# Performance work log

Measured on AMD Instinct MI355X. Metric: run time of the kernel, lower is better.

## Reference

```python
import jax, jax.numpy as jnp
import numpy as np

DC_WZ = 15
ETA = 0.1
RADIUS = DC_WZ // 2  # 7
EPS = 1e-3


def avg_pool2d(x, k, pad):
    # torch F.avg_pool2d default: zero padding, count_include_pad=True -> divide by k*k always
    s = jax.lax.reduce_window(
        x, 0.0, jax.lax.add,
        window_dimensions=(1, 1, k, k),
        window_strides=(1, 1, 1, 1),
        padding=[(0, 0), (0, 0), (pad, pad), (pad, pad)])
    return s / float(k * k)


def min_pool2d_replicate(x, k, pad):
    # replicate (edge) pad then VALID min-pool, matching -max_pool2d(-pad(x, replicate))
    xp = jnp.pad(x, ((0, 0), (0, 0), (pad, pad), (pad, pad)), mode='edge')
    return jax.lax.reduce_window(
        xp, jnp.inf, jax.lax.min,
        window_dimensions=(1, 1, k, k),
        window_strides=(1, 1, 1, 1),
        padding='VALID')


def guided_filter(guide, src, radius, eps=EPS):
    k = 2 * radius + 1
    mean_I = avg_pool2d(guide, k, radius)
    mean_p = avg_pool2d(src, k, radius)
    mean_Ip = avg_pool2d(guide * src, k, radius)
    cov_Ip = mean_Ip - mean_I * mean_p
    mean_II = avg_pool2d(guide * guide, k, radius)
    var_I = mean_II - mean_I * mean_I
    a = cov_Ip / (var_I + eps)
    b = mean_p - a * mean_I
    mean_a = avg_pool2d(a, k, radius)
    mean_b = avg_pool2d(b, k, radius)
    return mean_a * guide + mean_b


def setup_inputs() -> dict:
    key = jax.random.key(0)
    k1, k2 = jax.random.split(key)
    smoky_image = jax.random.uniform(k1, (16, 3, 512, 512), dtype=jnp.float32)
    rho_DNN = jax.random.uniform(k2, (16, 3, 512, 512), dtype=jnp.float32)
    return {"smoky_image": smoky_image, "rho_DNN": rho_DNN}


def reference(smoky_image, rho_DNN):
    # dark channel: per-pixel min over RGB, then 15x15 min-pool with replicate pad
    dc_pixel = jnp.min(smoky_image, axis=-3, keepdims=True)  # [B,1,H,W]
    dc_coarse = min_pool2d_replicate(dc_pixel, DC_WZ, RADIUS)
    guide_I = jnp.mean(smoky_image, axis=-3, keepdims=True)
    dc_refined = guided_filter(guide_I, dc_coarse, RADIUS, EPS)
    dc_refined = jax.lax.stop_gradient(dc_refined)  # torch: no_grad + detach
    dc_rho = (ETA + dc_refined) / (ETA + 1.0) * (1.0 - rho_DNN)
    return smoky_image - dc_rho
```

## Files before the change

kernel.cpp:

```cpp
#include <hip/hip_runtime.h>

#define BATCH 16
#define HH 512
#define WW 512
#define PLANE (HH*WW)

#define LDS_WAIT()   asm volatile("s_waitcnt lgkmcnt(0)" ::: "memory")
#define WAVE_FENCE() asm volatile("" ::: "memory")

__device__ __forceinline__ float bf_lo(unsigned u) {
    union { unsigned u; float f; } c; c.u = u << 16; return c.f;
}
__device__ __forceinline__ float bf_hi(unsigned u) {
    union { unsigned u; float f; } c; c.u = u & 0xFFFF0000u; return c.f;
}
__device__ __forceinline__ unsigned f2bf(float f) {
    union { float f; unsigned u; } c; c.f = f;
    return (c.u + 0x7FFFu + ((c.u >> 16) & 1u)) >> 16;
}
__device__ __forceinline__ unsigned packbf(float x, float y) {
    return f2bf(x) | (f2bf(y) << 16);
}
__device__ __forceinline__ float min3f(float a, float b, float c) {
    return fminf(fminf(a, b), c);
}

#define T1 64
#define HALO 7
#define LW (T1 + 2*HALO)

__global__ __launch_bounds__(256) void k1_guide_minpool(
    const float* __restrict__ smoky, unsigned* __restrict__ gp)
{
    __shared__ float dcp[LW*LW];
    __shared__ float vmn[T1*LW];
    __shared__ unsigned short gsh[T1*T1];
    int nwg = gridDim.x;
    int wg = (blockIdx.x & 7) * (nwg >> 3) + (blockIdx.x >> 3);
    int img  = wg >> 6;
    int tile = wg & 63;
    int y0 = (tile >> 3) * T1;
    int x0 = (tile & 7) * T1;
    int t = threadIdx.x;
    const float* s0 = smoky + (size_t)img * 3 * PLANE;
    unsigned* gpl = gp + (size_t)img * PLANE;

    for (int i = t; i < LW*LW; i += 256) {
        int ly = i / LW, lx = i - ly * LW;
        int iy = y0 - HALO + ly, ix = x0 - HALO + lx;
        int cy = min(max(iy, 0), HH-1);
        int cx = min(max(ix, 0), WW-1);
        const float* bp = s0 + cy * WW + cx;
        float c0 = bp[0], c1 = bp[PLANE], c2 = bp[2*PLANE];
        dcp[i] = min3f(c0, c1, c2);
        if (ly >= HALO && ly < HALO+T1 && lx >= HALO && lx < HALO+T1)
            gsh[(ly-HALO)*T1 + (lx-HALO)] = (unsigned short)f2bf((c0 + c1 + c2) * (1.0f/3.0f));
    }
    __syncthreads();
    for (int i = t; i < T1*LW; i += 256) {
        int r = i / LW, c = i - r * LW;
        const float* q = &dcp[r*LW + c];
        float m = min3f(min3f(min3f(q[0*LW],q[1*LW],q[2*LW]),
                              min3f(q[3*LW],q[4*LW],q[5*LW]),
                              min3f(q[6*LW],q[7*LW],q[8*LW])),
                        min3f(q[9*LW],q[10*LW],q[11*LW]),
                        min3f(q[12*LW],q[13*LW],q[14*LW]));
        vmn[i] = m;
    }
    __syncthreads();
    for (int i = t; i < T1*T1; i += 256) {
        int r = i >> 6, c = i & 63;
        const float* q = &vmn[r*LW + c];
        float m = min3f(min3f(min3f(q[0],q[1],q[2]),
                              min3f(q[3],q[4],q[5]),
                              min3f(q[6],q[7],q[8])),
                        min3f(q[9],q[10],q[11]),
                        min3f(q[12],q[13],q[14]));
        gpl[(y0+r)*WW + x0 + c] = (unsigned)gsh[r*T1+c] | (f2bf(m) << 16);
    }
}

#define RS2 8

__global__ __launch_bounds__(256) void k2_ab(
    const unsigned* __restrict__ gp, unsigned* __restrict__ abO)
{
    __shared__ float2 eo[4][4][80];
    int nwg = gridDim.x;
    int wg = (blockIdx.x & 7) * (nwg >> 3) + (blockIdx.x >> 3);
    int w = threadIdx.x >> 6, l = threadIdx.x & 63;
    int gw = wg * 4 + w;
    int img   = gw >> 8;
    int cg    = (gw >> 6) & 3;
    int strip = gw & 63;
    int y0 = strip * RS2;
    int c0 = cg * 128;
    const unsigned* gpP = gp + (size_t)img * PLANE;
    unsigned* abP = abO + (size_t)img * PLANE;

    int cm = c0 + 2*l;
    int hj = l & 3;
    int hcol  = (l < 4) ? (c0 - 8 + 2*hj) : (c0 + 128 + 2*hj);
    bool hv   = (l < 8) && (hcol >= 0) && (hcol < WW);
    int hslot = (l < 4) ? hj : (68 + hj);

    float sI[2]={0,0}, sII[2]={0,0}, sPv[2]={0,0}, sIp[2]={0,0};
    float hI[2]={0,0}, hII[2]={0,0}, hPv[2]={0,0}, hIp[2]={0,0};

    auto loadrow = [&](int y, uint2& um, uint2& uh) {
        int yc = min(max(y, 0), HH-1);
        const unsigned* r = gpP + (size_t)yc * WW;
        uint2 a = *reinterpret_cast<const uint2*>(r + cm);
        uint2 b = make_uint2(0u, 0u);
        if (hv) b = *reinterpret_cast<const uint2*>(r + hcol);
        bool rv = ((unsigned)y < (unsigned)HH);
        um.x = rv ? a.x : 0u;  um.y = rv ? a.y : 0u;
        uh.x = rv ? b.x : 0u;  uh.y = rv ? b.y : 0u;
    };

    for (int r = y0 - 8; r <= y0 + 6; ++r) {
        uint2 um, uh; loadrow(r, um, uh);
        unsigned mm[2]={um.x,um.y}, hh[2]={uh.x,uh.y};
        #pragma unroll
        for (int k = 0; k < 2; ++k) {
            float g=bf_lo(mm[k]), p=bf_hi(mm[k]);
            sI[k]+=g; sII[k]+=g*g; sPv[k]+=p; sIp[k]+=g*p;
            float gh=bf_lo(hh[k]), ph=bf_hi(hh[k]);
            hI[k]+=gh; hII[k]+=gh*gh; hPv[k]+=ph; hIp[k]+=gh*ph;
        }
    }
    uint2 adM, adH, sbM, sbH;
    loadrow(y0 + 7, adM, adH);
    loadrow(y0 - 8, sbM, sbH);

    float2* EO = &eo[w][0][0];
    const float inv225 = 1.0f/225.0f;
    for (int y = y0; y < y0 + RS2; ++y) {
        {
            unsigned am[2]={adM.x,adM.y}, sm[2]={sbM.x,sbM.y};
            unsigned ah[2]={adH.x,adH.y}, sh[2]={sbH.x,sbH.y};
            #pragma unroll
            for (int k = 0; k < 2; ++k) {
                float gA=bf_lo(am[k]), pA=bf_hi(am[k]);
                float gS=bf_lo(sm[k]), pS=bf_hi(sm[k]);
                sI[k]+=gA-gS; sII[k]+=gA*gA-gS*gS; sPv[k]+=pA-pS; sIp[k]+=gA*pA-gS*pS;
                float gAh=bf_lo(ah[k]), pAh=bf_hi(ah[k]);
                float gSh=bf_lo(sh[k]), pSh=bf_hi(sh[k]);
                hI[k]+=gAh-gSh; hII[k]+=gAh*gAh-gSh*gSh; hPv[k]+=pAh-pSh; hIp[k]+=gAh*pAh-gSh*pSh;
            }
        }
        loadrow(y + 8, adM, adH);
        loadrow(y - 7, sbM, sbH);
        EO[l+4]       = make_float2(sI[0],  sI[1]);
        EO[80 + l+4]  = make_float2(sII[0], sII[1]);
        EO[160 + l+4] = make_float2(sPv[0], sPv[1]);
        EO[240 + l+4] = make_float2(sIp[0], sIp[1]);
        if (l < 8) {
            EO[hslot]       = make_float2(hI[0],  hI[1]);
            EO[80 + hslot]  = make_float2(hII[0], hII[1]);
            EO[160 + hslot] = make_float2(hPv[0], hPv[1]);
            EO[240 + hslot] = make_float2(hIp[0], hIp[1]);
        }
        LDS_WAIT();
        float S0[4], S1[4];
        #pragma unroll
        for (int q = 0; q < 4; ++q) {
            float2 t[9];
            #pragma unroll
            for (int m = 0; m < 9; ++m) t[m] = EO[q*80 + l + m];
            float so = ((t[0].y+t[1].y)+(t[2].y+t[3].y)) + ((t[4].y+t[5].y)+(t[6].y+t[7].y));
            float se = ((t[1].x+t[2].x)+(t[3].x+t[4].x)) + ((t[5].x+t[6].x)+t[7].x);
            S0[q] = so + se;
            S1[q] = S0[q] - t[0].y + t[8].x;
        }
        WAVE_FENCE();
        unsigned pk0, pk1;
        {
            float mI = S0[0]*inv225, mP = S0[2]*inv225;
            float va = (S0[3]*inv225 - mI*mP) / (S0[1]*inv225 - mI*mI + 1e-3f);
            pk0 = packbf(va, mP - va*mI);
        }
        {
            float mI = S1[0]*inv225, mP = S1[2]*inv225;
            float va = (S1[3]*inv225 - mI*mP) / (S1[1]*inv225 - mI*mI + 1e-3f);
            pk1 = packbf(va, mP - va*mI);
        }
        *reinterpret_cast<uint2*>(abP + (size_t)y*WW + cm) = make_uint2(pk0, pk1);
    }
}

__global__ __launch_bounds__(256) void k3_final(
    const unsigned* __restrict__ abI,
    const float* __restrict__ smoky, const float* __restrict__ rho,
    float* __restrict__ out)
{
    __shared__ float2 eo[4][2][80];
    int nwg = gridDim.x;
    int wg = (blockIdx.x & 7) * (nwg >> 3) + (blockIdx.x >> 3);
    int w = threadIdx.x >> 6, l = threadIdx.x & 63;
    int gw = wg * 4 + w;
    int img   = gw >> 8;
    int cg    = (gw >> 6) & 3;
    int strip = gw & 63;
    int y0 = strip * RS2;
    int c0 = cg * 128;
    const unsigned* abP = abI + (size_t)img * PLANE;
    const float* sP = smoky + (size_t)img * 3 * PLANE;
    const float* rP = rho   + (size_t)img * 3 * PLANE;
    float* oP = out + (size_t)img * 3 * PLANE;

    int cm = c0 + 2*l;
    int hj = l & 3;
    int hcol  = (l < 4) ? (c0 - 8 + 2*hj) : (c0 + 128 + 2*hj);
    bool hv   = (l < 8) && (hcol >= 0) && (hcol < WW);
    int hslot = (l < 4) ? hj : (68 + hj);

    float sa[2]={0,0}, sb[2]={0,0}, ha[2]={0,0}, hb[2]={0,0};

    auto loadrow = [&](int y, uint2& um, uint2& uh) {
        int yc = min(max(y, 0), HH-1);
        const unsigned* r = abP + (size_t)yc * WW;
        uint2 a = *reinterpret_cast<const uint2*>(r + cm);
        uint2 b = make_uint2(0u, 0u);
        if (hv) b = *reinterpret_cast<const uint2*>(r + hcol);
        bool rv = ((unsigned)y < (unsigned)HH);
        um.x = rv ? a.x : 0u;  um.y = rv ? a.y : 0u;
        uh.x = rv ? b.x : 0u;  uh.y = rv ? b.y : 0u;
    };

    for (int r = y0 - 8; r <= y0 + 6; ++r) {
        uint2 um, uh; loadrow(r, um, uh);
        sa[0]+=bf_lo(um.x); sb[0]+=bf_hi(um.x);
        sa[1]+=bf_lo(um.y); sb[1]+=bf_hi(um.y);
        ha[0]+=bf_lo(uh.x); hb[0]+=bf_hi(uh.x);
        ha[1]+=bf_lo(uh.y); hb[1]+=bf_hi(uh.y);
    }
    uint2 adM, adH, sbM, sbH;
    loadrow(y0 + 7, adM, adH);
    loadrow(y0 - 8, sbM, sbH);

    float2 es0, es1, es2, er0, er1, er2;
    int yend = y0 + RS2;
    auto loademit = [&](int y) {
        int e = min(y, yend - 1);
        size_t off = (size_t)e*WW + cm;
        es0 = *reinterpret_cast<const float2*>(sP + off);
        es1 = *reinterpret_cast<const float2*>(sP + off + PLANE);
        es2 = *reinterpret_cast<const float2*>(sP + off + 2*PLANE);
        er0 = *reinterpret_cast<const float2*>(rP + off);
        er1 = *reinterpret_cast<const float2*>(rP + off + PLANE);
        er2 = *reinterpret_cast<const float2*>(rP + off + 2*PLANE);
    };
    loademit(y0);

    float2* EO = &eo[w][0][0];
    const float inv225 = 1.0f/225.0f;
    const float inv11  = 1.0f/1.1f;
    const float third  = 1.0f/3.0f;
    for (int y = y0; y < yend; ++y) {
        sa[0] += bf_lo(adM.x) - bf_lo(sbM.x);  sb[0] += bf_hi(adM.x) - bf_hi(sbM.x);
        sa[1] += bf_lo(adM.y) - bf_lo(sbM.y);  sb[1] += bf_hi(adM.y) - bf_hi(sbM.y);
        ha[0] += bf_lo(adH.x) - bf_lo(sbH.x);  hb[0] += bf_hi(adH.x) - bf_hi(sbH.x);
        ha[1] += bf_lo(adH.y) - bf_lo(sbH.y);  hb[1] += bf_hi(adH.y) - bf_hi(sbH.y);
        float2 cs0 = es0, cs1 = es1, cs2 = es2, cr0 = er0, cr1 = er1, cr2 = er2;
        loadrow(y + 8, adM, adH);
        loadrow(y - 7, sbM, sbH);
        loademit(y + 1);
        EO[l+4]      = make_float2(sa[0], sa[1]);
        EO[80 + l+4] = make_float2(sb[0], sb[1]);
        if (l < 8) {
            EO[hslot]      = make_float2(ha[0], ha[1]);
            EO[80 + hslot] = make_float2(hb[0], hb[1]);
        }
        LDS_WAIT();
        float SA0, SA1, SB0, SB1;
        {
            float2 t[9];
            #pragma unroll
            for (int m = 0; m < 9; ++m) t[m] = EO[l + m];
            float so = ((t[0].y+t[1].y)+(t[2].y+t[3].y)) + ((t[4].y+t[5].y)+(t[6].y+t[7].y));
            float se = ((t[1].x+t[2].x)+(t[3].x+t[4].x)) + ((t[5].x+t[6].x)+t[7].x);
            SA0 = so + se;  SA1 = SA0 - t[0].y + t[8].x;
        }
        {
            float2 t[9];
            #pragma unroll
            for (int m = 0; m < 9; ++m) t[m] = EO[80 + l + m];
            float so = ((t[0].y+t[1].y)+(t[2].y+t[3].y)) + ((t[4].y+t[5].y)+(t[6].y+t[7].y));
            float se = ((t[1].x+t[2].x)+(t[3].x+t[4].x)) + ((t[5].x+t[6].x)+t[7].x);
            SB0 = so + se;  SB1 = SB0 - t[0].y + t[8].x;
        }
        WAVE_FENCE();
        float g0 = (cs0.x + cs1.x + cs2.x) * third;
        float g1 = (cs0.y + cs1.y + cs2.y) * third;
        float f0 = (0.1f + SA0*inv225*g0 + SB0*inv225) * inv11;
        float f1 = (0.1f + SA1*inv225*g1 + SB1*inv225) * inv11;
        size_t off = (size_t)y*WW + cm;
        float2 o0, o1, o2;
        o0.x = cs0.x - f0*(1.0f - cr0.x);  o0.y = cs0.y - f1*(1.0f - cr0.y);
        o1.x = cs1.x - f0*(1.0f - cr1.x);  o1.y = cs1.y - f1*(1.0f - cr1.y);
        o2.x = cs2.x - f0*(1.0f - cr2.x);  o2.y = cs2.y - f1*(1.0f - cr2.y);
        *reinterpret_cast<float2*>(oP + off)           = o0;
        *reinterpret_cast<float2*>(oP + off + PLANE)   = o1;
        *reinterpret_cast<float2*>(oP + off + 2*PLANE) = o2;
    }
}

extern "C" void kernel_launch(void* const* d_in, const int* in_sizes, int n_in,
                              void* d_out, int out_size, void* d_ws, size_t ws_size,
                              hipStream_t stream) {
    const float* smoky = (const float*)d_in[0];
    const float* rho   = (const float*)d_in[1];
    float* out = (float*)d_out;
    const size_t P = (size_t)BATCH * PLANE;
    unsigned* gpbuf = (unsigned*)d_ws;
    unsigned* abbuf = (unsigned*)d_ws + P;

    k1_guide_minpool<<<BATCH*64, 256, 0, stream>>>(smoky, gpbuf);
    k2_ab<<<BATCH*64, 256, 0, stream>>>(gpbuf, abbuf);
    k3_final<<<BATCH*64, 256, 0, stream>>>(abbuf, smoky, rho, out);
}
```

Baseline: 81.38 us.

## Restructure final kernel into 64x64 LDS tiles with separable box sums

```diff
diff --git a/kernel.cpp b/kernel.cpp
--- a/kernel.cpp
+++ b/kernel.cpp
@@ -189,117 +189,110 @@
     }
 }
 
+#define T3 64
+#define AW 78
+#define VSW 82
+
 __global__ __launch_bounds__(256) void k3_final(
     const unsigned* __restrict__ abI,
     const float* __restrict__ smoky, const float* __restrict__ rho,
     float* __restrict__ out)
 {
-    __shared__ float2 eo[4][2][80];
+    __shared__ unsigned abt[AW*AW];
+    __shared__ float2 vs[T3*VSW];
     int nwg = gridDim.x;
     int wg = (blockIdx.x & 7) * (nwg >> 3) + (blockIdx.x >> 3);
-    int w = threadIdx.x >> 6, l = threadIdx.x & 63;
-    int gw = wg * 4 + w;
-    int img   = gw >> 8;
-    int cg    = (gw >> 6) & 3;
-    int strip = gw & 63;
-    int y0 = strip * RS2;
-    int c0 = cg * 128;
+    int img  = wg >> 6;
+    int tile = wg & 63;
+    int y0 = (tile >> 3) * T3;
+    int x0 = (tile & 7) * T3;
+    int t = threadIdx.x;
     const unsigned* abP = abI + (size_t)img * PLANE;
     const float* sP = smoky + (size_t)img * 3 * PLANE;
     const float* rP = rho   + (size_t)img * 3 * PLANE;
     float* oP = out + (size_t)img * 3 * PLANE;
 
-    int cm = c0 + 2*l;
-    int hj = l & 3;
-    int hcol  = (l < 4) ? (c0 - 8 + 2*hj) : (c0 + 128 + 2*hj);
-    bool hv   = (l < 8) && (hcol >= 0) && (hcol < WW);
-    int hslot = (l < 4) ? hj : (68 + hj);
-
-    float sa[2]={0,0}, sb[2]={0,0}, ha[2]={0,0}, hb[2]={0,0};
-
-    auto loadrow = [&](int y, uint2& um, uint2& uh) {
-        int yc = min(max(y, 0), HH-1);
-        const unsigned* r = abP + (size_t)yc * WW;
-        uint2 a = *reinterpret_cast<const uint2*>(r + cm);
-        uint2 b = make_uint2(0u, 0u);
-        if (hv) b = *reinterpret_cast<const uint2*>(r + hcol);
-        bool rv = ((unsigned)y < (unsigned)HH);
-        um.x = rv ? a.x : 0u;  um.y = rv ? a.y : 0u;
-        uh.x = rv ? b.x : 0u;  uh.y = rv ? b.y : 0u;
-    };
-
-    for (int r = y0 - 8; r <= y0 + 6; ++r) {
-        uint2 um, uh; loadrow(r, um, uh);
-        sa[0]+=bf_lo(um.x); sb[0]+=bf_hi(um.x);
-        sa[1]+=bf_lo(um.y); sb[1]+=bf_hi(um.y);
-        ha[0]+=bf_lo(uh.x); hb[0]+=bf_hi(uh.x);
-        ha[1]+=bf_lo(uh.y); hb[1]+=bf_hi(uh.y);
-    }
-    uint2 adM, adH, sbM, sbH;
-    loadrow(y0 + 7, adM, adH);
-    loadrow(y0 - 8, sbM, sbH);
-
-    float2 es0, es1, es2, er0, er1, er2;
-    int yend = y0 + RS2;
-    auto loademit = [&](int y) {
-        int e = min(y, yend - 1);
-        size_t off = (size_t)e*WW + cm;
-        es0 = *reinterpret_cast<const float2*>(sP + off);
-        es1 = *reinterpret_cast<const float2*>(sP + off + PLANE);
-        es2 = *reinterpret_cast<const float2*>(sP + off + 2*PLANE);
-        er0 = *reinterpret_cast<const float2*>(rP + off);
-        er1 = *reinterpret_cast<const float2*>(rP + off + PLANE);
-        er2 = *reinterpret_cast<const float2*>(rP + off + 2*PLANE);
-    };
-    loademit(y0);
-
-    float2* EO = &eo[w][0][0];
-    const float inv225 = 1.0f/225.0f;
-    const float inv11  = 1.0f/1.1f;
-    const float third  = 1.0f/3.0f;
-    for (int y = y0; y < yend; ++y) {
-        sa[0] += bf_lo(adM.x) - bf_lo(sbM.x);  sb[0] += bf_hi(adM.x) - bf_hi(sbM.x);
-        sa[1] += bf_lo(adM.y) - bf_lo(sbM.y);  sb[1] += bf_hi(adM.y) - bf_hi(sbM.y);
-        ha[0] += bf_lo(adH.x) - bf_lo(sbH.x);  hb[0] += bf_hi(adH.x) - bf_hi(sbH.x);
-        ha[1] += bf_lo(adH.y) - bf_lo(sbH.y);  hb[1] += bf_hi(adH.y) - bf_hi(sbH.y);
-        float2 cs0 = es0, cs1 = es1, cs2 = es2, cr0 = er0, cr1 = er1, cr2 = er2;
-        loadrow(y + 8, adM, adH);
-        loadrow(y - 7, sbM, sbH);
-        loademit(y + 1);
-        EO[l+4]      = make_float2(sa[0], sa[1]);
-        EO[80 + l+4] = make_float2(sb[0], sb[1]);
-        if (l < 8) {
-            EO[hslot]      = make_float2(ha[0], ha[1]);
-            EO[80 + hslot] = make_float2(hb[0], hb[1]);
-        }
-        LDS_WAIT();
-        float SA0, SA1, SB0, SB1;
+    for (int i = t; i < AW*AW; i += 256) {
+        int ly = i / AW, lx = i - ly * AW;
+        int gy = y0 - 7 + ly, gx = x0 - 7 + lx;
+        unsigned v = 0u;
+        if ((unsigned)gy < (unsigned)HH && (unsigned)gx < (unsigned)WW)
+            v = abP[(size_t)gy * WW + gx];
+        abt[i] = v;
+    }
+    __syncthreads();
+
+    if (t < 234) {
+        int rb = (t >= 156) ? 2 : (t >= 78 ? 1 : 0);
+        int c  = t - rb * 78;
+        int r0 = (rb == 0) ? 0 : (rb == 1 ? 22 : 43);
+        int r1 = (rb == 0) ? 21 : (rb == 1 ? 42 : 63);
+        float sA = 0.f, sB = 0.f;
+        #pragma unroll
+        for (int k = 0; k < 15; ++k) {
+            unsigned u = abt[(r0 + k)*AW + c];
+            sA += bf_lo(u); sB += bf_hi(u);
+        }
+        vs[r0*VSW + c] = make_float2(sA, sB);
+        for (int r = r0 + 1; r <= r1; ++r) {
+            unsigned ua = abt[(r + 14)*AW + c];
+            unsigned us = abt[(r - 1)*AW + c];
+            sA += bf_lo(ua) - bf_lo(us);
+            sB += bf_hi(ua) - bf_hi(us);
+            vs[r*VSW + c] = make_float2(sA, sB);
+        }
+    }
+    __syncthreads();
+
+    unsigned* m = abt;
+    {
+        int r = t >> 2, g = t & 3;
+        const float2* vr = &vs[r*VSW + g*16];
+        const float inv225 = 1.0f/225.0f;
+        float SA, SB;
         {
-            float2 t[9];
-            #pragma unroll
-            for (int m = 0; m < 9; ++m) t[m] = EO[l + m];
-            float so = ((t[0].y+t[1].y)+(t[2].y+t[3].y)) + ((t[4].y+t[5].y)+(t[6].y+t[7].y));
-            float se = ((t[1].x+t[2].x)+(t[3].x+t[4].x)) + ((t[5].x+t[6].x)+t[7].x);
-            SA0 = so + se;  SA1 = SA0 - t[0].y + t[8].x;
-        }
-        {
-            float2 t[9];
-            #pragma unroll
-            for (int m = 0; m < 9; ++m) t[m] = EO[80 + l + m];
-            float so = ((t[0].y+t[1].y)+(t[2].y+t[3].y)) + ((t[4].y+t[5].y)+(t[6].y+t[7].y));
-            float se = ((t[1].x+t[2].x)+(t[3].x+t[4].x)) + ((t[5].x+t[6].x)+t[7].x);
-            SB0 = so + se;  SB1 = SB0 - t[0].y + t[8].x;
-        }
-        WAVE_FENCE();
-        float g0 = (cs0.x + cs1.x + cs2.x) * third;
-        float g1 = (cs0.y + cs1.y + cs2.y) * third;
-        float f0 = (0.1f + SA0*inv225*g0 + SB0*inv225) * inv11;
-        float f1 = (0.1f + SA1*inv225*g1 + SB1*inv225) * inv11;
-        size_t off = (size_t)y*WW + cm;
+            float2 a0=vr[0], a1=vr[1], a2=vr[2], a3=vr[3], a4=vr[4], a5=vr[5], a6=vr[6], a7=vr[7];
+            float2 a8=vr[8], a9=vr[9], a10=vr[10], a11=vr[11], a12=vr[12], a13=vr[13], a14=vr[14];
+            SA = (((a0.x+a1.x)+(a2.x+a3.x)) + ((a4.x+a5.x)+(a6.x+a7.x)))
+               + (((a8.x+a9.x)+(a10.x+a11.x)) + ((a12.x+a13.x)+a14.x));
+            SB = (((a0.y+a1.y)+(a2.y+a3.y)) + ((a4.y+a5.y)+(a6.y+a7.y)))
+               + (((a8.y+a9.y)+(a10.y+a11.y)) + ((a12.y+a13.y)+a14.y));
+        }
+        m[r*64 + g*16] = packbf(SA*inv225, SB*inv225);
+        #pragma unroll
+        for (int j = 1; j < 16; ++j) {
+            float2 ua = vr[14 + j];
+            float2 us = vr[j - 1];
+            SA += ua.x - us.x;
+            SB += ua.y - us.y;
+            m[r*64 + g*16 + j] = packbf(SA*inv225, SB*inv225);
+        }
+    }
+    __syncthreads();
+
+    const float inv11 = 1.0f/1.1f;
+    const float third = 1.0f/3.0f;
+    #pragma unroll
+    for (int it = 0; it < 8; ++it) {
+        int i2 = it*256 + t;
+        int r  = i2 >> 5;
+        int cp = (i2 & 31) * 2;
+        size_t off = (size_t)(y0 + r)*WW + x0 + cp;
+        float2 s0 = *reinterpret_cast<const float2*>(sP + off);
+        float2 s1 = *reinterpret_cast<const float2*>(sP + off + PLANE);
+        float2 s2 = *reinterpret_cast<const float2*>(sP + off + 2*PLANE);
+        float2 r0 = *reinterpret_cast<const float2*>(rP + off);
+        float2 r1 = *reinterpret_cast<const float2*>(rP + off + PLANE);
+        float2 r2 = *reinterpret_cast<const float2*>(rP + off + 2*PLANE);
+        unsigned m0 = m[r*64 + cp], m1 = m[r*64 + cp + 1];
+        float g0 = (s0.x + s1.x + s2.x) * third;
+        float g1 = (s0.y + s1.y + s2.y) * third;
+        float q0 = (0.1f + bf_lo(m0)*g0 + bf_hi(m0)) * inv11;
+        float q1 = (0.1f + bf_lo(m1)*g1 + bf_hi(m1)) * inv11;
         float2 o0, o1, o2;
-        o0.x = cs0.x - f0*(1.0f - cr0.x);  o0.y = cs0.y - f1*(1.0f - cr0.y);
-        o1.x = cs1.x - f0*(1.0f - cr1.x);  o1.y = cs1.y - f1*(1.0f - cr1.y);
-        o2.x = cs2.x - f0*(1.0f - cr2.x);  o2.y = cs2.y - f1*(1.0f - cr2.y);
+        o0.x = s0.x - q0*(1.0f - r0.x);  o0.y = s0.y - q1*(1.0f - r0.y);
+        o1.x = s1.x - q0*(1.0f - r1.x);  o1.y = s1.y - q1*(1.0f - r1.y);
+        o2.x = s2.x - q0*(1.0f - r2.x);  o2.y = s2.y - q1*(1.0f - r2.y);
         *reinterpret_cast<float2*>(oP + off)           = o0;
         *reinterpret_cast<float2*>(oP + off + PLANE)   = o1;
         *reinterpret_cast<float2*>(oP + off + 2*PLANE) = o2;
```

New measurement: 92.55 us. +13.7%, slower.
